# Optimization experiments

Measured on AMD Instinct MI355X. Metric: run time of the kernel, lower is better.

The kernel has to match this reference:

```python
import jax, jax.numpy as jnp
import numpy as np

NUM_METAPATHS = 3
ETYPES = np.array([[0, 1], [2, 3], [4, 5]])  # [P, L-1], indices into expanded r_vec
N_NODES = 100000
N_TARGETS = 8192
E = 250000
L = 3
IN_DIM = 64
NUM_HEADS = 8
ATTN_VEC_DIM = 128
OUT_DIM = 64
ALPHA = 0.01  # LeakyReLU slope


def setup_inputs() -> dict:
    key = jax.random.key(0)
    ks = jax.random.split(key, 10)
    features = jax.random.normal(ks[0], (N_NODES, IN_DIM), jnp.float32)
    indices = jax.random.randint(ks[1], (NUM_METAPATHS, E, L), 0, N_NODES)
    dst = jax.random.randint(ks[2], (NUM_METAPATHS, E), 0, N_TARGETS)
    r_vec = jax.random.normal(ks[3], (3, IN_DIM // 2, 2), jnp.float32) * 0.5
    attn = jax.random.normal(ks[4], (NUM_METAPATHS, NUM_HEADS, IN_DIM), jnp.float32) * 0.1
    fc1_w = jax.random.normal(ks[5], (ATTN_VEC_DIM, IN_DIM * NUM_HEADS), jnp.float32) * 0.05
    fc1_b = jnp.zeros((ATTN_VEC_DIM,), jnp.float32)
    fc2_w = jax.random.normal(ks[6], (1, ATTN_VEC_DIM), jnp.float32) * 0.1
    fc_w = jax.random.normal(ks[7], (OUT_DIM, IN_DIM * NUM_HEADS), jnp.float32) * 0.05
    fc_b = jnp.zeros((OUT_DIM,), jnp.float32)
    return dict(features=features, indices=indices, dst=dst, r_vec=r_vec, attn=attn,
                fc1_w=fc1_w, fc1_b=fc1_b, fc2_w=fc2_w, fc_w=fc_w, fc_b=fc_b)


def _cmul(a, b):
    # complex multiply on trailing [..., 2] (real, imag) pairs
    re = a[..., 0] * b[..., 0] - a[..., 1] * b[..., 1]
    im = a[..., 0] * b[..., 1] + a[..., 1] * b[..., 0]
    return jnp.stack([re, im], axis=-1)


def _final_r_vec(r_full):
    # r_full: [num_edge_type, d2, 2] -> cumulative rotations per metapath [P, L, d2, 2]
    d2 = r_full.shape[1]
    one = jnp.stack([jnp.ones((d2,), r_full.dtype), jnp.zeros((d2,), r_full.dtype)], axis=-1)
    finals = []
    for p in range(NUM_METAPATHS):
        f = [None] * L
        f[L - 1] = one
        for i in range(L - 2, -1, -1):
            f[i] = _cmul(f[i + 1], r_full[int(ETYPES[p, i])])
        finals.append(jnp.stack(f))
    return jnp.stack(finals)  # [P, L, d2, 2]


def _forward(features, indices, dst, r_vec, attn, fc1_w, fc1_b, fc2_w, fc_w, fc_b):
    d2 = IN_DIM // 2
    # RotatE0: L2-normalize each complex rotation, then expand with conjugates
    r = r_vec / jnp.sqrt(jnp.sum(r_vec * r_vec, axis=-1, keepdims=True))
    r_conj = r * jnp.array([1.0, -1.0], r.dtype)
    r_full = jnp.stack([r, r_conj], axis=1).reshape(-1, d2, 2)  # [num_edge_type, d2, 2]
    final_r = _final_r_vec(r_full)  # [P, L, d2, 2]; final[L-1] = 1+0j (identity)

    def per_metapath(idx, d_idx, final_rv, attn_p):
        # idx: [E, L] node ids, d_idx: [E] destination (target) ids
        edata = features[idx].reshape(E, L, d2, 2)           # gather metapath instances
        edata = _cmul(edata, final_rv[None])                 # rotate each position
        hidden = edata.reshape(E, L, IN_DIM).mean(axis=1)    # [E, d]
        eft = jnp.broadcast_to(hidden[:, None, :], (E, NUM_HEADS, IN_DIM))
        a = jnp.einsum('ehd,hd->eh', eft, attn_p)
        a = jnp.where(a > 0, a, ALPHA * a)                   # leaky_relu
        # edge softmax per destination segment (stable)
        a_max = jax.ops.segment_max(a, d_idx, num_segments=N_TARGETS)
        a = jnp.exp(a - a_max[d_idx])
        a_sum = jax.ops.segment_sum(a, d_idx, num_segments=N_TARGETS)
        a = a / a_sum[d_idx]
        ft = jax.ops.segment_sum(eft * a[:, :, None], d_idx, num_segments=N_TARGETS)
        return ft.reshape(N_TARGETS, NUM_HEADS * IN_DIM)

    outs = jax.vmap(per_metapath)(indices, dst, final_r, attn)  # [P, Nt, H*d]
    outs = jax.nn.elu(outs)
    # inter-metapath attention
    fc1 = jnp.tanh(jnp.einsum('pnd,ad->pna', outs, fc1_w) + fc1_b)  # [P, Nt, A]
    beta = fc1.mean(axis=1) @ fc2_w.T                               # [P, 1]
    beta = jax.nn.softmax(beta[:, 0])                               # [P]
    h = jnp.einsum('p,pnd->nd', beta, outs)                         # [Nt, H*d]
    h_fc = h @ fc_w.T + fc_b                                        # [Nt, out_dim]
    return h_fc, h


def reference(features, indices, dst, r_vec, attn, fc1_w, fc1_b, fc2_w, fc_w, fc_b):
    return _forward(features, indices, dst, r_vec, attn, fc1_w, fc1_b, fc2_w, fc_w, fc_b)
```

## Files before the change

### kernel.cpp

```cpp
#include <hip/hip_runtime.h>
#include <hip/hip_bf16.h>
#include <hip/hip_fp16.h>

#define NP   3
#define NE   250000
#define NL   3
#define NT   8192
#define NN   100000
#define IND  64
#define ND2  32
#define NH   8
#define NAD  128
#define NOD  64
#define NHD  512
#define LALPHA 0.01f
#define NSEG (NP*NT)
#define NB   16

typedef __attribute__((ext_vector_type(8))) _Float16 half8;
typedef __attribute__((ext_vector_type(4))) _Float16 half4;
typedef __attribute__((ext_vector_type(4))) float f32x4;
typedef __attribute__((ext_vector_type(4))) unsigned int uint4v;

#define FLAG_W    0
#define FINALR_W  64
#define ATILDE_W  704
#define BETAACC_N 5376
#define BETA_N    5760
#define COUNTS_N  6144
#define OFFS_N    30720
#define CURSOR_N  55360
#define EIDX_N    80000
#define ATTNF_N   3080000
#define FC1W_N    3081600
#define FC1B_N    3147136
#define FC2W_N    3147264
#define FCW_N     3147392
#define FCB_N     3180160
#define RVEC_N    3180224
#define FEATH_N   3180544
#define SCORE_N   6380544
#define OUTS_N    13580544
#define EH_N      19872000
#define NEED_WORDS 25872000UL

#define BETAACC_F 1024
#define BETA_F    1472
#define COUNTS_F  2048
#define OFFS_F    26624
#define CURSOR_F  51264
#define ELIST_F   75904
#define FEATF_F   825920
#define ATTNF_F   7225920
#define FC1W_F    7227456
#define FC1B_F    7292992
#define FC2W_F    7293120
#define FCW_F     7293248
#define FCB_F     7326016
#define RVEC_F    7326080
#define OUTS_F    7326272

__device__ __forceinline__ float bf2f(unsigned short u) {
    union { unsigned int i; float f; } c; c.i = ((unsigned int)u) << 16; return c.f;
}

__device__ __forceinline__ void fmamix_lo(float& acc, unsigned int xpair, float s) {
    asm("v_fma_mix_f32 %0, %1, %2, %0 op_sel_hi:[1,0,0]"
        : "+v"(acc) : "v"(xpair), "v"(s));
}
__device__ __forceinline__ void fmamix_hi(float& acc, unsigned int xpair, float s) {
    asm("v_fma_mix_f32 %0, %1, %2, %0 op_sel:[1,0,0] op_sel_hi:[1,0,0]"
        : "+v"(acc) : "v"(xpair), "v"(s));
}

__global__ __launch_bounds__(256) void k_prep(
        const unsigned short* __restrict__ feat_raw,
        const void* __restrict__ rvec_src, const void* __restrict__ attn_src,
        const void* __restrict__ fc1b_src, const void* __restrict__ fc2w_src,
        const void* __restrict__ fcb_src,
        float* __restrict__ ws, int* __restrict__ flag,
        float* __restrict__ rvecf, float* __restrict__ attnf,
        float* __restrict__ fc1bf, float* __restrict__ fc2wf,
        float* __restrict__ fcbf) {
    __shared__ int cnt;
    int t = threadIdx.x;
    if (t == 0) cnt = 0;
    __syncthreads();
    int wild = 0;
    for (int i = t; i < 512; i += 256) {
        unsigned short u = feat_raw[i];
        int e = (u >> 7) & 0xFF;
        if (u != 0 && (e < 0x60 || e > 0x90)) wild++;
    }
    for (int off = 32; off; off >>= 1) wild += __shfl_xor(wild, off);
    if ((t & 63) == 0) atomicAdd(&cnt, wild);
    __syncthreads();
    int f = cnt > 64 ? 1 : 0;
    if (t == 0) *flag = f;
    for (int i = t; i < 192; i += 256)
        rvecf[i] = f ? ((const float*)rvec_src)[i] : bf2f(((const unsigned short*)rvec_src)[i]);
    for (int i = t; i < 1536; i += 256)
        attnf[i] = f ? ((const float*)attn_src)[i] : bf2f(((const unsigned short*)attn_src)[i]);
    if (t < 128) fc1bf[t] = f ? ((const float*)fc1b_src)[t] : bf2f(((const unsigned short*)fc1b_src)[t]);
    if (t < 128) fc2wf[t] = f ? ((const float*)fc2w_src)[t] : bf2f(((const unsigned short*)fc2w_src)[t]);
    if (t < 64)  fcbf[t]  = f ? ((const float*)fcb_src)[t]  : bf2f(((const unsigned short*)fcb_src)[t]);
    __syncthreads();
    if (t < NP * ND2) {
        int p = t / ND2, j = t % ND2;
        float re = rvecf[(p * ND2 + j) * 2 + 0];
        float im = rvecf[(p * ND2 + j) * 2 + 1];
        float inv = rsqrtf(re * re + im * im);
        float nre = re * inv, nim = im * inv;
        float f1r = nre, f1i = -nim;
        float f0r = f1r * nre - f1i * nim;
        float f0i = f1r * nim + f1i * nre;
        float* fr = ws + FINALR_W + p * NL * ND2 * 2;
        fr[(0 * ND2 + j) * 2 + 0] = f0r; fr[(0 * ND2 + j) * 2 + 1] = f0i;
        fr[(1 * ND2 + j) * 2 + 0] = f1r; fr[(1 * ND2 + j) * 2 + 1] = f1i;
        fr[(2 * ND2 + j) * 2 + 0] = 1.f; fr[(2 * ND2 + j) * 2 + 1] = 0.f;
    }
    __syncthreads();
    const float* finalr = ws + FINALR_W;
    float* atil = ws + ATILDE_W;
    for (int i = t; i < NP * NL * NH * IND; i += 256) {
        int d = i & 63, h = (i >> 6) & 7, l = (i >> 9) % 3, p = i / (64 * 8 * 3);
        int j = d >> 1; bool im = (d & 1) != 0;
        float cr = finalr[(p * NL * ND2 + l * ND2 + j) * 2 + 0];
        float ci = finalr[(p * NL * ND2 + l * ND2 + j) * 2 + 1];
        float ar = attnf[(p * NH + h) * IND + 2 * j];
        float ai = attnf[(p * NH + h) * IND + 2 * j + 1];
        float v = im ? (ai * cr - ar * ci) : (ar * cr + ai * ci);
        atil[i] = v * (1.f / 3.f);
    }
}

__global__ void k_cvt(const void* __restrict__ src, float* __restrict__ dst, int n,
                      const int* __restrict__ flag) {
    int i = blockIdx.x * blockDim.x + threadIdx.x;
    if (i >= n) return;
    if (*flag) dst[i] = ((const float*)src)[i];
    else       dst[i] = bf2f(((const unsigned short*)src)[i]);
}

__global__ void k_cvt_h4(const void* __restrict__ src, half4* __restrict__ dst, int n4,
                         const int* __restrict__ flag) {
    int i = blockIdx.x * blockDim.x + threadIdx.x;
    if (i >= n4) return;
    half4 o;
    if (*flag) {
        float4 v = ((const float4*)src)[i];
        o[0] = (_Float16)v.x; o[1] = (_Float16)v.y; o[2] = (_Float16)v.z; o[3] = (_Float16)v.w;
    } else {
        ushort4 u = ((const ushort4*)src)[i];
        o[0] = (_Float16)bf2f(u.x); o[1] = (_Float16)bf2f(u.y);
        o[2] = (_Float16)bf2f(u.z); o[3] = (_Float16)bf2f(u.w);
    }
    dst[i] = o;
}

__global__ void k_cvt_tr(const void* __restrict__ src, float* __restrict__ dst,
                         int R, int C, const int* __restrict__ flag) {
    int i = blockIdx.x * blockDim.x + threadIdx.x;
    if (i >= R * C) return;
    int r = i / C, c = i % C;
    float v;
    if (*flag) v = ((const float*)src)[i];
    else       v = bf2f(((const unsigned short*)src)[i]);
    dst[c * R + r] = v;
}

__global__ __launch_bounds__(256) void k_score(const void* __restrict__ feat_src,
                                               const int* __restrict__ flag,
                                               const float* __restrict__ atil,
                                               float* __restrict__ S,
                                               _Float16* __restrict__ featH) {
    __shared__ float xs[128][68];
    __shared__ float as[72][68];
    int t = threadIdx.x;
    int nbase = blockIdx.x * 128;
    int f = *flag;
    for (int i = t; i < 72 * 64; i += 256) as[i >> 6][i & 63] = atil[i];
    for (int c = t; c < 2048; c += 256) {
        int nloc = c >> 4, cc = c & 15;
        int node = nbase + nloc;
        float4 v;
        if (node < NN) {
            if (f) v = ((const float4*)feat_src)[(size_t)node * 16 + cc];
            else {
                ushort4 u = ((const ushort4*)feat_src)[(size_t)node * 16 + cc];
                v = make_float4(bf2f(u.x), bf2f(u.y), bf2f(u.z), bf2f(u.w));
            }
        } else v = make_float4(0.f, 0.f, 0.f, 0.f);
        int d0 = cc * 4;
        xs[nloc][d0 + 0] = v.x; xs[nloc][d0 + 1] = v.y;
        xs[nloc][d0 + 2] = v.z; xs[nloc][d0 + 3] = v.w;
        if (node < NN) {
            half4 hv;
            hv[0] = (_Float16)v.x; hv[1] = (_Float16)v.y;
            hv[2] = (_Float16)v.z; hv[3] = (_Float16)v.w;
            *(half4*)(featH + (size_t)node * IND + d0) = hv;
        }
    }
    __syncthreads();
    int lane = t & 63, w = t >> 6;
    int g = lane >> 3, h = lane & 7;
    int nloc = (w * 8 + g) * 4;
    float acc[9][4];
#pragma unroll
    for (int c = 0; c < 9; c++)
#pragma unroll
        for (int u = 0; u < 4; u++) acc[c][u] = 0.f;
    for (int ch = 0; ch < 16; ch++) {
        float4 xv[4];
#pragma unroll
        for (int u = 0; u < 4; u++) xv[u] = *(const float4*)&xs[nloc + u][ch * 4];
#pragma unroll
        for (int c = 0; c < 9; c++) {
            float4 av = *(const float4*)&as[c * 8 + h][ch * 4];
#pragma unroll
            for (int u = 0; u < 4; u++)
                acc[c][u] += xv[u].x * av.x + xv[u].y * av.y + xv[u].z * av.z + xv[u].w * av.w;
        }
    }
#pragma unroll
    for (int u = 0; u < 4; u++) {
        int node = nbase + nloc + u;
        if (node < NN) {
#pragma unroll
            for (int c = 0; c < 9; c++)
                S[(long)node * 72 + c * 8 + h] = acc[c][u];
        }
    }
}

__global__ void k_count(const int* __restrict__ dst, int* __restrict__ counts) {
    int id = blockIdx.x * blockDim.x + threadIdx.x;
    if (id >= NP * NE) return;
    int p = id / NE;
    atomicAdd(&counts[p * NT + dst[id]], 1);
}

__global__ __launch_bounds__(256) void k_scan(const int* __restrict__ counts,
                                              int* __restrict__ offs,
                                              int* __restrict__ cursor) {
    __shared__ int wtot[4];
    int t = threadIdx.x;
    const int CH = NSEG / 256;
    int base = t * CH;
    int s = 0;
    for (int i = 0; i < CH; i++) s += counts[base + i];
    int l = t & 63, w = t >> 6;
    int v = s;
    for (int off = 1; off < 64; off <<= 1) {
        int u = __shfl_up(v, off);
        if (l >= off) v += u;
    }
    if (l == 63) wtot[w] = v;
    __syncthreads();
    int wb = 0;
    for (int i = 0; i < w; i++) wb += wtot[i];
    int run = wb + v - s;
    for (int i = 0; i < CH; i++) {
        int c = counts[base + i];
        offs[base + i] = run; cursor[base + i] = run;
        run += c;
    }
    if (t == 255) offs[NSEG] = wb + v;
}

__global__ void k_scatter2(const int* __restrict__ dst, const int* __restrict__ indices,
                           int* __restrict__ cursor, int4* __restrict__ eidx,
                           const float* __restrict__ S, float* __restrict__ EH) {
    int id = blockIdx.x * blockDim.x + threadIdx.x;
    if (id >= NP * NE) return;
    int p = id / NE, e = id % NE;
    int pos = atomicAdd(&cursor[p * NT + dst[id]], 1);
    const int* ip = indices + (long)p * NE * NL + (long)e * NL;
    int n0 = ip[0], n1 = ip[1], n2 = ip[2];
    eidx[pos] = make_int4(n0, n1, n2, 0);
    const float* S0 = S + (long)n0 * 72 + p * 24;
    const float* S1 = S + (long)n1 * 72 + p * 24 + 8;
    const float* S2 = S + (long)n2 * 72 + p * 24 + 16;
    float4 a0 = *(const float4*)S0, b0 = *(const float4*)(S0 + 4);
    float4 a1 = *(const float4*)S1, b1 = *(const float4*)(S1 + 4);
    float4 a2 = *(const float4*)S2, b2 = *(const float4*)(S2 + 4);
    float4 lo, hi;
    {
        float s;
        s = a0.x + a1.x + a2.x; lo.x = __expf(fmaxf(s, LALPHA * s));
        s = a0.y + a1.y + a2.y; lo.y = __expf(fmaxf(s, LALPHA * s));
        s = a0.z + a1.z + a2.z; lo.z = __expf(fmaxf(s, LALPHA * s));
        s = a0.w + a1.w + a2.w; lo.w = __expf(fmaxf(s, LALPHA * s));
        s = b0.x + b1.x + b2.x; hi.x = __expf(fmaxf(s, LALPHA * s));
        s = b0.y + b1.y + b2.y; hi.y = __expf(fmaxf(s, LALPHA * s));
        s = b0.z + b1.z + b2.z; hi.z = __expf(fmaxf(s, LALPHA * s));
        s = b0.w + b1.w + b2.w; hi.w = __expf(fmaxf(s, LALPHA * s));
    }
    float* ehp = EH + (long)pos * 8;
    *(float4*)ehp = lo;
    *(float4*)(ehp + 4) = hi;
}

__global__ void k_scatter(const int* __restrict__ dst, int* __restrict__ cursor,
                          int* __restrict__ elist) {
    int id = blockIdx.x * blockDim.x + threadIdx.x;
    if (id >= NP * NE) return;
    int p = id / NE, e = id % NE;
    int pos = atomicAdd(&cursor[p * NT + dst[id]], 1);
    elist[pos] = e;
}

__global__ __launch_bounds__(64) void k_agg2(
        const _Float16* __restrict__ featH, const int4* __restrict__ eidx,
        const float* __restrict__ EH, const float* __restrict__ finalr,
        const int* __restrict__ offs, _Float16* __restrict__ outs) {
    int b = blockIdx.x;
    int p = b / NT;
    int t = threadIdx.x;
    int h = t >> 3, q = t & 7;

    float a0[8], a1[8], a2[8];
#pragma unroll
    for (int r = 0; r < 8; r++) { a0[r] = 0.f; a1[r] = 0.f; a2[r] = 0.f; }
    float se = 0.f;

    int beg = offs[b], end = offs[b + 1];
    const float* EHh = EH + h;

    int i = beg;
    for (; i + 4 <= end; i += 4) {
        int4 ee[4];
        float ehv[4];
        half8 x0[4], x1[4], x2[4];
#pragma unroll
        for (int u = 0; u < 4; u++) ehv[u] = EHh[(long)(i + u) * 8];
#pragma unroll
        for (int u = 0; u < 4; u++) ee[u] = eidx[i + u];
#pragma unroll
        for (int u = 0; u < 4; u++) {
            x0[u] = *(const half8*)(featH + ((long)ee[u].x << 6) + (q << 3));
            x1[u] = *(const half8*)(featH + ((long)ee[u].y << 6) + (q << 3));
            x2[u] = *(const half8*)(featH + ((long)ee[u].z << 6) + (q << 3));
        }
#pragma unroll
        for (int u = 0; u < 4; u++) {
            float eh = ehv[u];
            se += eh;
            uint4v w0 = __builtin_bit_cast(uint4v, x0[u]);
            uint4v w1 = __builtin_bit_cast(uint4v, x1[u]);
            uint4v w2 = __builtin_bit_cast(uint4v, x2[u]);
#pragma unroll
            for (int jp = 0; jp < 4; jp++) {
                fmamix_lo(a0[2 * jp], w0[jp], eh); fmamix_hi(a0[2 * jp + 1], w0[jp], eh);
                fmamix_lo(a1[2 * jp], w1[jp], eh); fmamix_hi(a1[2 * jp + 1], w1[jp], eh);
                fmamix_lo(a2[2 * jp], w2[jp], eh); fmamix_hi(a2[2 * jp + 1], w2[jp], eh);
            }
        }
    }
    for (; i < end; i++) {
        int4 e = eidx[i];
        float eh = EHh[(long)i * 8];
        se += eh;
        half8 x0 = *(const half8*)(featH + ((long)e.x << 6) + (q << 3));
        half8 x1 = *(const half8*)(featH + ((long)e.y << 6) + (q << 3));
        half8 x2 = *(const half8*)(featH + ((long)e.z << 6) + (q << 3));
#pragma unroll
        for (int r = 0; r < 8; r++) {
            a0[r] += eh * (float)x0[r];
            a1[r] += eh * (float)x1[r];
            a2[r] += eh * (float)x2[r];
        }
    }

    const float* fr = finalr + p * NL * ND2 * 2;
    float sc = (end > beg) ? (1.f / 3.f) / se : 0.f;
    half8 o;
#pragma unroll
    for (int jj = 0; jj < 4; jj++) {
        int j = 4 * q + jj;
        float c0r = fr[(0 * ND2 + j) * 2 + 0], c0i = fr[(0 * ND2 + j) * 2 + 1];
        float c1r = fr[(1 * ND2 + j) * 2 + 0], c1i = fr[(1 * ND2 + j) * 2 + 1];
        float ar, ai, vr, vi;
        ar = a0[2 * jj]; ai = a0[2 * jj + 1];
        vr = ar * c0r - ai * c0i; vi = ar * c0i + ai * c0r;
        ar = a1[2 * jj]; ai = a1[2 * jj + 1];
        vr += ar * c1r - ai * c1i; vi += ar * c1i + ai * c1r;
        vr += a2[2 * jj]; vi += a2[2 * jj + 1];
        vr *= sc; vi *= sc;
        vr = vr > 0.f ? vr : __expf(vr) - 1.f;
        vi = vi > 0.f ? vi : __expf(vi) - 1.f;
        o[2 * jj]     = (_Float16)vr;
        o[2 * jj + 1] = (_Float16)vi;
    }
    *(half8*)(outs + (long)b * NHD + (h << 6) + (q << 3)) = o;
}

__global__ __launch_bounds__(64) void k_agg(
        const float* __restrict__ feat, const int* __restrict__ indices,
        const float* __restrict__ attn, const float* __restrict__ ws_f,
        const int* __restrict__ offs, const int* __restrict__ elist,
        _Float16* __restrict__ outs) {
    int b = blockIdx.x;
    int p = b / NT;
    int d = threadIdx.x;
    int j = d >> 1;
    bool isim = (d & 1) != 0;
    const float* fr = ws_f + FINALR_W + p * NL * ND2 * 2;
    float cr[NL], ci[NL];
#pragma unroll
    for (int l = 0; l < NL; l++) {
        cr[l] = fr[(l * ND2 + j) * 2 + 0];
        ci[l] = fr[(l * ND2 + j) * 2 + 1];
    }
    float at[NH];
#pragma unroll
    for (int h = 0; h < NH; h++) at[h] = attn[(p * NH + h) * IND + d];
    float ft[NH], se[NH];
#pragma unroll
    for (int h = 0; h < NH; h++) { ft[h] = 0.f; se[h] = 0.f; }
    int beg = offs[b], end = offs[b + 1];
    const int* idxp = indices + (long)p * NE * NL;
    for (int i = beg; i < end; i++) {
        int e = elist[i];
        int nn[3] = { idxp[e * 3 + 0], idxp[e * 3 + 1], idxp[e * 3 + 2] };
        float hid = 0.f;
#pragma unroll
        for (int l = 0; l < NL; l++) {
            float x = feat[(long)nn[l] * IND + d];
            float xp = __shfl_xor(x, 1);
            float re = isim ? xp : x;
            float im = isim ? x : xp;
            hid += isim ? (re * ci[l] + im * cr[l]) : (re * cr[l] - im * ci[l]);
        }
        hid *= (1.f / 3.f);
#pragma unroll
        for (int h = 0; h < NH; h++) {
            float v = hid * at[h];
#pragma unroll
            for (int off = 32; off; off >>= 1) v += __shfl_xor(v, off);
            float a = v > 0.f ? v : LALPHA * v;
            float eh = __expf(a);
            se[h] += eh;
            ft[h] += eh * hid;
        }
    }
    _Float16* orow = outs + (long)b * NHD;
    bool has = end > beg;
#pragma unroll
    for (int h = 0; h < NH; h++) {
        float v = has ? ft[h] / fmaxf(se[h], 1e-20f) : 0.f;
        v = v > 0.f ? v : (__expf(v) - 1.f);
        orow[h * IND + d] = (_Float16)v;
    }
}

__global__ __launch_bounds__(256) void k_fc1(
        const _Float16* __restrict__ outs, const _Float16* __restrict__ fc1h,
        const float* __restrict__ fc1_b, float* __restrict__ betaacc) {
    __shared__ float red[4][NAD];
    int tid = threadIdx.x;
    int wid = tid >> 6, lane = tid & 63;
    int nt = blockIdx.x * 4 + wid;
    int p  = blockIdx.x / (NT / 16 / 4);
    int col = lane & 15, kq = lane >> 4;

    const _Float16* brow  = outs + ((long)nt * 16 + col) * NHD + kq * 8;
    const _Float16* abase = fc1h + (long)col * NHD + kq * 8;

    f32x4 acc[8];
#pragma unroll
    for (int ta = 0; ta < 8; ta++) acc[ta] = (f32x4){0.f, 0.f, 0.f, 0.f};

    for (int kk = 0; kk < 16; kk++) {
        half8 b = *(const half8*)(brow + kk * 32);
#pragma unroll
        for (int ta = 0; ta < 8; ta++) {
            half8 a = *(const half8*)(abase + (long)ta * 16 * NHD + kk * 32);
            acc[ta] = __builtin_amdgcn_mfma_f32_16x16x32_f16(a, b, acc[ta], 0, 0, 0);
        }
    }

#pragma unroll
    for (int ta = 0; ta < 8; ta++) {
#pragma unroll
        for (int r = 0; r < 4; r++) {
            int arow = ta * 16 + kq * 4 + r;
            float v = tanhf(acc[ta][r] + fc1_b[arow]);
            v += __shfl_xor(v, 1); v += __shfl_xor(v, 2);
            v += __shfl_xor(v, 4); v += __shfl_xor(v, 8);
            if (col == 0) red[wid][arow] = v;
        }
    }
    __syncthreads();
    if (tid < NAD) {
        float s = red[0][tid] + red[1][tid] + red[2][tid] + red[3][tid];
        atomicAdd(&betaacc[p * NAD + tid], s);
    }
}

__global__ void k_beta(const float* __restrict__ betaacc,
                       const float* __restrict__ fc2_w, float* __restrict__ beta) {
    __shared__ float lds[NP][NAD];
    int t = threadIdx.x;
    for (int p = 0; p < NP; p++)
        lds[p][t] = betaacc[p * NAD + t] * (1.f / NT) * fc2_w[t];
    __syncthreads();
    if (t == 0) {
        float s[NP];
        for (int p = 0; p < NP; p++) {
            s[p] = 0.f;
            for (int a = 0; a < NAD; a++) s[p] += lds[p][a];
        }
        float m = fmaxf(s[0], fmaxf(s[1], s[2]));
        float e0 = expf(s[0] - m), e1 = expf(s[1] - m), e2 = expf(s[2] - m);
        float inv = 1.f / (e0 + e1 + e2);
        beta[0] = e0 * inv; beta[1] = e1 * inv; beta[2] = e2 * inv;
    }
}

__global__ __launch_bounds__(256) void k_final(
        const _Float16* __restrict__ outs, const float* __restrict__ beta,
        const float* __restrict__ fc_wT, const float* __restrict__ fc_b,
        void* __restrict__ outp, const int* __restrict__ flag) {
    __shared__ float h[NB * NHD];
    __shared__ float part[4 * NB * NOD];
    int n0 = blockIdx.x * NB;
    int t = threadIdx.x;
    int f = *flag;
    float b0 = beta[0], b1 = beta[1], b2 = beta[2];
    const _Float16* o0 = outs + (long)n0 * NHD;
    for (int i = t; i < NB * NHD / 8; i += 256) {
        half8 v0 = *(const half8*)(o0 + i * 8);
        half8 v1 = *(const half8*)(o0 + (long)NT * NHD + i * 8);
        half8 v2 = *(const half8*)(o0 + 2L * NT * NHD + i * 8);
#pragma unroll
        for (int jj = 0; jj < 8; jj++) {
            float v = b0 * (float)v0[jj] + b1 * (float)v1[jj] + b2 * (float)v2[jj];
            h[i * 8 + jj] = v;
            long idx = (long)NT * NOD + (long)n0 * NHD + i * 8 + jj;
            if (f) ((float*)outp)[idx] = v;
            else   ((__hip_bfloat16*)outp)[idx] = __float2bfloat16(v);
        }
    }
    __syncthreads();
    int w = t >> 6, l = t & 63;
    float acc[NB];
#pragma unroll
    for (int n = 0; n < NB; n++) acc[n] = 0.f;
    for (int k = w * 128; k < (w + 1) * 128; k++) {
        float wv = fc_wT[k * NOD + l];
#pragma unroll
        for (int n = 0; n < NB; n++) acc[n] += h[n * NHD + k] * wv;
    }
#pragma unroll
    for (int n = 0; n < NB; n++) part[(w * NB + n) * NOD + l] = acc[n];
    __syncthreads();
    for (int idx = t; idx < NB * NOD; idx += 256) {
        int n = idx >> 6, ll = idx & 63;
        float v = part[(0 * NB + n) * NOD + ll] + part[(1 * NB + n) * NOD + ll]
                + part[(2 * NB + n) * NOD + ll] + part[(3 * NB + n) * NOD + ll]
                + fc_b[ll];
        long oidx = (long)(n0 + n) * NOD + ll;
        if (f) ((float*)outp)[oidx] = v;
        else   ((__hip_bfloat16*)outp)[oidx] = __float2bfloat16(v);
    }
}

extern "C" void kernel_launch(void* const* d_in, const int* in_sizes, int n_in,
                              void* d_out, int out_size, void* d_ws, size_t ws_size,
                              hipStream_t stream) {
    const int* indices = (const int*)d_in[1];
    const int* dst     = (const int*)d_in[2];

    float* ws  = (float*)d_ws;
    int*   wsi = (int*)d_ws;

    bool big = ws_size >= NEED_WORDS * 4UL;

    const int betaacc = big ? BETAACC_N : BETAACC_F;
    const int beta    = big ? BETA_N    : BETA_F;
    const int counts  = big ? COUNTS_N  : COUNTS_F;
    const int offs    = big ? OFFS_N    : OFFS_F;
    const int cursor  = big ? CURSOR_N  : CURSOR_F;
    const int attnf   = big ? ATTNF_N   : ATTNF_F;
    const int fc1w    = big ? FC1W_N    : FC1W_F;
    const int fc1b    = big ? FC1B_N    : FC1B_F;
    const int fc2w    = big ? FC2W_N    : FC2W_F;
    const int fcw     = big ? FCW_N     : FCW_F;
    const int fcb     = big ? FCB_N     : FCB_F;
    const int rvec    = big ? RVEC_N    : RVEC_F;
    const int outsw   = big ? OUTS_N    : OUTS_F;
    _Float16* outsp = (_Float16*)(ws + outsw);
    _Float16* fc1h  = (_Float16*)(ws + fc1w);

    hipMemsetAsync((char*)d_ws + (size_t)counts * 4, 0, NSEG * 4, stream);
    hipMemsetAsync((char*)d_ws + (size_t)betaacc * 4, 0, NP * NAD * 4, stream);

    k_prep<<<1, 256, 0, stream>>>((const unsigned short*)d_in[0],
                                  d_in[3], d_in[4], d_in[6], d_in[7], d_in[9],
                                  ws, wsi + FLAG_W,
                                  ws + rvec, ws + attnf, ws + fc1b, ws + fc2w,
                                  ws + fcb);

    k_cvt_h4<<<(NAD * NHD / 4 + 255) / 256, 256, 0, stream>>>(d_in[5], (half4*)fc1h,
                                                              NAD * NHD / 4, wsi + FLAG_W);
    k_cvt_tr<<<(NOD * NHD + 255) / 256, 256, 0, stream>>>(d_in[8], ws + fcw,
                                                          NOD, NHD, wsi + FLAG_W);
    k_count<<<(NP * NE + 255) / 256, 256, 0, stream>>>(dst, wsi + counts);
    k_scan<<<1, 256, 0, stream>>>(wsi + counts, wsi + offs, wsi + cursor);

    if (big) {
        _Float16* featH = (_Float16*)(ws + FEATH_N);
        k_score<<<(NN + 127) / 128, 256, 0, stream>>>(d_in[0], wsi + FLAG_W,
                                                      ws + ATILDE_W, ws + SCORE_N, featH);
        k_scatter2<<<(NP * NE + 255) / 256, 256, 0, stream>>>(dst, indices,
                                                              wsi + cursor,
                                                              (int4*)(wsi + EIDX_N),
                                                              ws + SCORE_N, ws + EH_N);
        k_agg2<<<NSEG, 64, 0, stream>>>(featH, (const int4*)(wsi + EIDX_N),
                                        ws + EH_N, ws + FINALR_W,
                                        wsi + offs, outsp);
    } else {
        k_cvt<<<(NN * IND + 255) / 256, 256, 0, stream>>>(d_in[0], ws + FEATF_F,
                                                          NN * IND, wsi + FLAG_W);
        k_scatter<<<(NP * NE + 255) / 256, 256, 0, stream>>>(dst, wsi + cursor,
                                                             wsi + ELIST_F);
        k_agg<<<NSEG, 64, 0, stream>>>(ws + FEATF_F, indices, ws + attnf, ws,
                                       wsi + offs, wsi + ELIST_F, outsp);
    }

    k_fc1<<<NP * NT / 16 / 4, 256, 0, stream>>>(outsp, fc1h, ws + fc1b, ws + betaacc);
    k_beta<<<1, 128, 0, stream>>>(ws + betaacc, ws + fc2w, ws + beta);
    k_final<<<NT / NB, 256, 0, stream>>>(outsp, ws + beta, ws + fcw, ws + fcb,
                                         d_out, wsi + FLAG_W);
}
```

Measured before the change: 320.8 us.

## Use MFMA for final FC, store pre-shifted byte offsets in edge index

The final projection kernel now stages the beta-weighted rows as fp16 in shared memory and computes h @ fc_w^T with 16x16x32 f16 MFMA instructions, replacing the scalar fp32 loop. This drops the transposed fp32 weight conversion kernel in favour of the existing fp16 converter. Separately, the scatter kernel stores node indices pre-shifted to byte offsets, so the aggregation kernel does 32-bit address arithmetic instead of 64-bit. The risks are fp16 rounding of h in the projection and 32-bit offset overflow if the feature table ever grows past 4 GB.

```diff
diff --git a/kernel.cpp b/kernel.cpp
--- a/kernel.cpp
+++ b/kernel.cpp
@@ -156,17 +156,6 @@
         o[2] = (_Float16)bf2f(u.z); o[3] = (_Float16)bf2f(u.w);
     }
     dst[i] = o;
-}
-
-__global__ void k_cvt_tr(const void* __restrict__ src, float* __restrict__ dst,
-                         int R, int C, const int* __restrict__ flag) {
-    int i = blockIdx.x * blockDim.x + threadIdx.x;
-    if (i >= R * C) return;
-    int r = i / C, c = i % C;
-    float v;
-    if (*flag) v = ((const float*)src)[i];
-    else       v = bf2f(((const unsigned short*)src)[i]);
-    dst[c * R + r] = v;
 }
 
 __global__ __launch_bounds__(256) void k_score(const void* __restrict__ feat_src,
@@ -277,7 +266,7 @@
     int pos = atomicAdd(&cursor[p * NT + dst[id]], 1);
     const int* ip = indices + (long)p * NE * NL + (long)e * NL;
     int n0 = ip[0], n1 = ip[1], n2 = ip[2];
-    eidx[pos] = make_int4(n0, n1, n2, 0);
+    eidx[pos] = make_int4(n0 << 7, n1 << 7, n2 << 7, 0);
     const float* S0 = S + (long)n0 * 72 + p * 24;
     const float* S1 = S + (long)n1 * 72 + p * 24 + 8;
     const float* S2 = S + (long)n2 * 72 + p * 24 + 16;
@@ -318,6 +307,8 @@
     int p = b / NT;
     int t = threadIdx.x;
     int h = t >> 3, q = t & 7;
+    const unsigned fB = (unsigned)(q << 4);
+    const char* Fb = (const char*)featH;
 
     float a0[8], a1[8], a2[8];
 #pragma unroll
@@ -338,9 +329,9 @@
         for (int u = 0; u < 4; u++) ee[u] = eidx[i + u];
 #pragma unroll
         for (int u = 0; u < 4; u++) {
-            x0[u] = *(const half8*)(featH + ((long)ee[u].x << 6) + (q << 3));
-            x1[u] = *(const half8*)(featH + ((long)ee[u].y << 6) + (q << 3));
-            x2[u] = *(const half8*)(featH + ((long)ee[u].z << 6) + (q << 3));
+            x0[u] = *(const half8*)(Fb + (unsigned)((unsigned)ee[u].x + fB));
+            x1[u] = *(const half8*)(Fb + (unsigned)((unsigned)ee[u].y + fB));
+            x2[u] = *(const half8*)(Fb + (unsigned)((unsigned)ee[u].z + fB));
         }
 #pragma unroll
         for (int u = 0; u < 4; u++) {
@@ -361,9 +352,9 @@
         int4 e = eidx[i];
         float eh = EHh[(long)i * 8];
         se += eh;
-        half8 x0 = *(const half8*)(featH + ((long)e.x << 6) + (q << 3));
-        half8 x1 = *(const half8*)(featH + ((long)e.y << 6) + (q << 3));
-        half8 x2 = *(const half8*)(featH + ((long)e.z << 6) + (q << 3));
+        half8 x0 = *(const half8*)(Fb + (unsigned)((unsigned)e.x + fB));
+        half8 x1 = *(const half8*)(Fb + (unsigned)((unsigned)e.y + fB));
+        half8 x2 = *(const half8*)(Fb + (unsigned)((unsigned)e.z + fB));
 #pragma unroll
         for (int r = 0; r < 8; r++) {
             a0[r] += eh * (float)x0[r];
@@ -520,47 +511,45 @@
 
 __global__ __launch_bounds__(256) void k_final(
         const _Float16* __restrict__ outs, const float* __restrict__ beta,
-        const float* __restrict__ fc_wT, const float* __restrict__ fc_b,
+        const _Float16* __restrict__ fcw16, const float* __restrict__ fc_b,
         void* __restrict__ outp, const int* __restrict__ flag) {
-    __shared__ float h[NB * NHD];
-    __shared__ float part[4 * NB * NOD];
+    __shared__ _Float16 h16[16][520];
     int n0 = blockIdx.x * NB;
     int t = threadIdx.x;
     int f = *flag;
     float b0 = beta[0], b1 = beta[1], b2 = beta[2];
     const _Float16* o0 = outs + (long)n0 * NHD;
-    for (int i = t; i < NB * NHD / 8; i += 256) {
-        half8 v0 = *(const half8*)(o0 + i * 8);
-        half8 v1 = *(const half8*)(o0 + (long)NT * NHD + i * 8);
-        half8 v2 = *(const half8*)(o0 + 2L * NT * NHD + i * 8);
+    for (int c = t; c < NB * NHD / 8; c += 256) {
+        int row = c >> 6, k0 = (c & 63) * 8;
+        half8 v0 = *(const half8*)(o0 + row * NHD + k0);
+        half8 v1 = *(const half8*)(o0 + (long)NT * NHD + row * NHD + k0);
+        half8 v2 = *(const half8*)(o0 + 2L * NT * NHD + row * NHD + k0);
+        half8 hv;
 #pragma unroll
         for (int jj = 0; jj < 8; jj++) {
             float v = b0 * (float)v0[jj] + b1 * (float)v1[jj] + b2 * (float)v2[jj];
-            h[i * 8 + jj] = v;
-            long idx = (long)NT * NOD + (long)n0 * NHD + i * 8 + jj;
+            hv[jj] = (_Float16)v;
+            long idx = (long)NT * NOD + (long)(n0 + row) * NHD + k0 + jj;
             if (f) ((float*)outp)[idx] = v;
             else   ((__hip_bfloat16*)outp)[idx] = __float2bfloat16(v);
         }
-    }
-    __syncthreads();
-    int w = t >> 6, l = t & 63;
-    float acc[NB];
-#pragma unroll
-    for (int n = 0; n < NB; n++) acc[n] = 0.f;
-    for (int k = w * 128; k < (w + 1) * 128; k++) {
-        float wv = fc_wT[k * NOD + l];
-#pragma unroll
-        for (int n = 0; n < NB; n++) acc[n] += h[n * NHD + k] * wv;
-    }
-#pragma unroll
-    for (int n = 0; n < NB; n++) part[(w * NB + n) * NOD + l] = acc[n];
-    __syncthreads();
-    for (int idx = t; idx < NB * NOD; idx += 256) {
-        int n = idx >> 6, ll = idx & 63;
-        float v = part[(0 * NB + n) * NOD + ll] + part[(1 * NB + n) * NOD + ll]
-                + part[(2 * NB + n) * NOD + ll] + part[(3 * NB + n) * NOD + ll]
-                + fc_b[ll];
-        long oidx = (long)(n0 + n) * NOD + ll;
+        *(half8*)&h16[row][k0] = hv;
+    }
+    __syncthreads();
+    int w = t >> 6, lane = t & 63;
+    int col = lane & 15, kq = lane >> 4;
+    const _Float16* abase = fcw16 + (long)(w * 16 + col) * NHD + kq * 8;
+    f32x4 acc = (f32x4){0.f, 0.f, 0.f, 0.f};
+    for (int kk = 0; kk < 16; kk++) {
+        half8 bfrag = *(const half8*)&h16[col][kq * 8 + kk * 32];
+        half8 afrag = *(const half8*)(abase + kk * 32);
+        acc = __builtin_amdgcn_mfma_f32_16x16x32_f16(afrag, bfrag, acc, 0, 0, 0);
+    }
+#pragma unroll
+    for (int r = 0; r < 4; r++) {
+        int arow = w * 16 + kq * 4 + r;
+        float v = acc[r] + fc_b[arow];
+        long oidx = (long)(n0 + col) * NOD + arow;
         if (f) ((float*)outp)[oidx] = v;
         else   ((__hip_bfloat16*)outp)[oidx] = __float2bfloat16(v);
     }
@@ -592,6 +581,7 @@
     const int outsw   = big ? OUTS_N    : OUTS_F;
     _Float16* outsp = (_Float16*)(ws + outsw);
     _Float16* fc1h  = (_Float16*)(ws + fc1w);
+    _Float16* fcw16 = (_Float16*)(ws + fcw);
 
     hipMemsetAsync((char*)d_ws + (size_t)counts * 4, 0, NSEG * 4, stream);
     hipMemsetAsync((char*)d_ws + (size_t)betaacc * 4, 0, NP * NAD * 4, stream);
@@ -604,8 +594,8 @@
 
     k_cvt_h4<<<(NAD * NHD / 4 + 255) / 256, 256, 0, stream>>>(d_in[5], (half4*)fc1h,
                                                               NAD * NHD / 4, wsi + FLAG_W);
-    k_cvt_tr<<<(NOD * NHD + 255) / 256, 256, 0, stream>>>(d_in[8], ws + fcw,
-                                                          NOD, NHD, wsi + FLAG_W);
+    k_cvt_h4<<<(NOD * NHD / 4 + 255) / 256, 256, 0, stream>>>(d_in[8], (half4*)fcw16,
+                                                              NOD * NHD / 4, wsi + FLAG_W);
     k_count<<<(NP * NE + 255) / 256, 256, 0, stream>>>(dst, wsi + counts);
     k_scan<<<1, 256, 0, stream>>>(wsi + counts, wsi + offs, wsi + cursor);
 
@@ -631,6 +621,6 @@
 
     k_fc1<<<NP * NT / 16 / 4, 256, 0, stream>>>(outsp, fc1h, ws + fc1b, ws + betaacc);
     k_beta<<<1, 128, 0, stream>>>(ws + betaacc, ws + fc2w, ws + beta);
-    k_final<<<NT / NB, 256, 0, stream>>>(outsp, ws + beta, ws + fcw, ws + fcb,
+    k_final<<<NT / NB, 256, 0, stream>>>(outsp, ws + beta, fcw16, ws + fcb,
                                          d_out, wsi + FLAG_W);
 }
```

Result: faster. 310.4 us (-3.2%).
